# Kernel tuning notes

Measured on AMD Instinct MI355X. Metric: run time of the kernel, lower is better.

## Reference

```python
import jax, jax.numpy as jnp
import numpy as np

# qint16 range and intermediate reciprocal scale (from Div.__init__):
# table_scale = 2 / 0.01 / (qmax - qmin) -> max representable ~ 1/0.01 = 100
QMIN, QMAX = -32768.0, 32767.0
TABLE_SCALE = 2.0 / 0.01 / 65535.0
N_TABLE = 256  # entries per LUT
DENSE = (0.01, 1.0)
SPARSE = (1.0, 7.0)
LLINE = (1e-5, 0.01)
RLINE = (7.0, 20.0)


def _quant(y):
    # quantize a float reciprocal value into the symmetric qint16 table domain
    return jnp.clip(jnp.round(y / TABLE_SCALE), QMIN, QMAX)


def _build_table(xmin, xmax):
    xs = jnp.linspace(xmin, xmax, N_TABLE, dtype=jnp.float32)
    return _quant(1.0 / xs)  # [N_TABLE] quantized reciprocal values


def _lookup(table, ax, xmin, xmax):
    step = (xmax - xmin) / (N_TABLE - 1)
    idx = jnp.clip(jnp.round((ax - xmin) / step), 0, N_TABLE - 1).astype(jnp.int32)
    return table[idx]


def _line(ax, x0, x1):
    # linear fit of reciprocal between the two segment endpoints, then quantize
    y0, y1 = 1.0 / x0, 1.0 / x1
    return _quant(y0 + (ax - x0) * (y1 - y0) / (x1 - x0))


def setup_inputs() -> dict:
    key = jax.random.key(0)
    k1, k2 = jax.random.split(key)
    shape = (4, 16, 1024, 1024)
    data1_q = jax.random.randint(k1, shape, -32768, 32768, dtype=jnp.int32)
    data2_q = jax.random.randint(k2, shape, -32768, 32768, dtype=jnp.int32)
    return {
        "data1_q": data1_q,
        "data2_q": data2_q,
        "data1_scale": jnp.array(1e-3, dtype=jnp.float32),
        "data2_scale": jnp.array(2e-4, dtype=jnp.float32),
        "out_scale": jnp.array(1e-3, dtype=jnp.float32),
    }


def reference(data1_q, data2_q, data1_scale, data2_scale, out_scale):
    # --- multi-table reciprocal on dequantized divisor (symmetric) ---
    x2 = data2_q.astype(jnp.float32) * data2_scale
    sign = jnp.where(x2 >= 0.0, 1.0, -1.0)
    ax = jnp.abs(x2)

    dense_t = _build_table(*DENSE)
    sparse_t = _build_table(*SPARSE)

    recip_q = jnp.where(
        ax < LLINE[0], _quant(1.0 / LLINE[0]),                  # left constant (saturates)
        jnp.where(ax < DENSE[0], _line(ax, *LLINE),             # left line segment
        jnp.where(ax < SPARSE[0], _lookup(dense_t, ax, *DENSE), # dense table
        jnp.where(ax < RLINE[0], _lookup(sparse_t, ax, *SPARSE),# sparse table
        jnp.where(ax < RLINE[1], _line(ax, *RLINE),             # right line segment
                  _quant(1.0 / RLINE[1]))))))                    # right constant
    recip_q = sign * recip_q  # symmetric extension, zero_point = 0

    # --- quantized mul: (data1 * reciprocal) requantized to out_scale ---
    prod = data1_q.astype(jnp.float32) * data1_scale * (recip_q * TABLE_SCALE)
    out_q = jnp.clip(jnp.round(prod / out_scale), QMIN, QMAX)
    return out_q  # int16 repr of QTensor(out_q, out_scale, 'qint16'), as float32
```

## Files before the change

### kernel.cpp

```cpp
#include <hip/hip_runtime.h>


#define TS64     (2.0 / 0.01 / 65535.0)
#define STEPD    (0.99 / 255.0)
#define STEPS    (6.0 / 255.0)
#define INVSTEPD (1.0 / (0.99 / 255.0))
#define INVSTEPS (1.0 / (6.0 / 255.0))

__device__ __forceinline__ void build_tables(double* tbl) {
    const int t = threadIdx.x;
    if (t < 256) {
        double pd = (double)t * STEPD;
        double ps = (double)t * STEPS;
        asm volatile("" : "+v"(pd));
        asm volatile("" : "+v"(ps));
        double xd = 0.01 + pd;
        double xs = 1.0 + ps;
        if (t == 255) { xd = 1.0; xs = 7.0; }
        double qd = rint((1.0 / xd) / TS64);
        double qs = rint((1.0 / xs) / TS64);
        tbl[t]       = fmin(fmax(qd, -32768.0), 32767.0);
        tbl[t + 256] = fmin(fmax(qs, -32768.0), 32767.0);
    }
    __syncthreads();
}

__device__ __forceinline__ float div_elem(int q1i, int q2i, double s2d, double Kd,
                                          const double* tbl) {
    const double ax = fabs((double)q2i * s2d);
    const bool dense = ax < 1.0;
    const double xmin = dense ? 0.01 : 1.0;
    const double inv  = dense ? INVSTEPD : INVSTEPS;
    double idxd = rint((ax - xmin) * inv);
    idxd = fmin(fmax(idxd, 0.0), 255.0);
    double rq = tbl[(int)idxd + (dense ? 0 : 256)];

    if (__builtin_expect(!(ax >= 0.01 && ax < 7.0), 0)) {
        if (ax < 0.01) {
            rq = 32767.0;
        } else if (ax < 20.0) {
            const double y0 = 1.0 / 7.0;
            const double dy = 0.05 - 1.0 / 7.0;
            double y = y0 + (ax - 7.0) * dy / 13.0;
            rq = fmin(fmax(rint(y / TS64), -32768.0), 32767.0);
        } else {
            rq = 16.0;
        }
    }
    rq = (q2i < 0) ? -rq : rq;
    double o = rint((double)q1i * Kd * rq);
    o = fmin(fmax(o, -32768.0), 32767.0);
    return (float)o;
}

__global__ void __launch_bounds__(256)
div_q16_vec4(const int4* __restrict__ q1, const int4* __restrict__ q2,
             const float* __restrict__ s1p, const float* __restrict__ s2p,
             const float* __restrict__ osp, float4* __restrict__ out, int nvec) {
    __shared__ double tbl[512];
    build_tables(tbl);
    const double s2d = (double)s2p[0];
    const double Kd  = (double)s1p[0] * TS64 / (double)osp[0];
    const int stride = gridDim.x * blockDim.x;
    for (int i = blockIdx.x * blockDim.x + threadIdx.x; i < nvec; i += stride) {
        const int4 a = q1[i];
        const int4 b = q2[i];
        float4 o;
        o.x = div_elem(a.x, b.x, s2d, Kd, tbl);
        o.y = div_elem(a.y, b.y, s2d, Kd, tbl);
        o.z = div_elem(a.z, b.z, s2d, Kd, tbl);
        o.w = div_elem(a.w, b.w, s2d, Kd, tbl);
        out[i] = o;
    }
}

__global__ void __launch_bounds__(256)
div_q16_tail(const int* __restrict__ q1, const int* __restrict__ q2,
             const float* __restrict__ s1p, const float* __restrict__ s2p,
             const float* __restrict__ osp, float* __restrict__ out,
             int base, int n) {
    __shared__ double tbl[512];
    build_tables(tbl);
    const double s2d = (double)s2p[0];
    const double Kd  = (double)s1p[0] * TS64 / (double)osp[0];
    const int i = base + blockIdx.x * (int)blockDim.x + threadIdx.x;
    if (i < n) out[i] = div_elem(q1[i], q2[i], s2d, Kd, tbl);
}

extern "C" void kernel_launch(void* const* d_in, const int* in_sizes, int n_in,
                              void* d_out, int out_size, void* d_ws, size_t ws_size,
                              hipStream_t stream) {
    const int n = in_sizes[0];
    const int* q1 = (const int*)d_in[0];
    const int* q2 = (const int*)d_in[1];
    const float* s1 = (const float*)d_in[2];
    const float* s2 = (const float*)d_in[3];
    const float* os = (const float*)d_in[4];
    float* out = (float*)d_out;

    const int nvec = n >> 2;
    const int block = 256;
    if (nvec > 0) {
        int grid = (nvec + block - 1) / block;
        if (grid > 2048) grid = 2048;
        div_q16_vec4<<<grid, block, 0, stream>>>(
            (const int4*)q1, (const int4*)q2, s1, s2, os, (float4*)out, nvec);
    }
    const int tail = n & 3;
    if (tail) {
        div_q16_tail<<<1, block, 0, stream>>>(q1, q2, s1, s2, os, out,
                                              n - tail, n);
    }
}
```

Measured before the change: 163.8 us.

## Replace per-element reciprocal evaluation with per-block 32K-entry integer-indexed LUT

Each block now builds a 32768-entry ushort LDS table that maps |q2| straight to the quantized reciprocal. The per-element fp64 arithmetic (dense/sparse index computation, line segments) becomes one LDS load, and the requantize multiply drops to fp32. Each block pays for building a 64KB table, computing 32 entries per thread in fp64 with a division. Block size goes to 1024 and the grid is capped at 512, which lowers occupancy. Using fp32 for the product may round some results differently from the fp64 path.

```diff
diff --git a/kernel.cpp b/kernel.cpp
--- a/kernel.cpp
+++ b/kernel.cpp
@@ -1,90 +1,88 @@
 #include <hip/hip_runtime.h>
 
 
-#define TS64     (2.0 / 0.01 / 65535.0)
-#define STEPD    (0.99 / 255.0)
-#define STEPS    (6.0 / 255.0)
-#define INVSTEPD (1.0 / (0.99 / 255.0))
-#define INVSTEPS (1.0 / (6.0 / 255.0))
+#define TS64  (2.0 / 0.01 / 65535.0)
+#define STEPD (0.99 / 255.0)
+#define STEPS (6.0 / 255.0)
 
-__device__ __forceinline__ void build_tables(double* tbl) {
-    const int t = threadIdx.x;
-    if (t < 256) {
-        double pd = (double)t * STEPD;
-        double ps = (double)t * STEPS;
-        asm volatile("" : "+v"(pd));
-        asm volatile("" : "+v"(ps));
-        double xd = 0.01 + pd;
-        double xs = 1.0 + ps;
-        if (t == 255) { xd = 1.0; xs = 7.0; }
-        double qd = rint((1.0 / xd) / TS64);
-        double qs = rint((1.0 / xs) / TS64);
-        tbl[t]       = fmin(fmax(qd, -32768.0), 32767.0);
-        tbl[t + 256] = fmin(fmax(qs, -32768.0), 32767.0);
+__device__ __forceinline__ double quant64(double y) {
+    return fmin(fmax(rint(y / TS64), -32768.0), 32767.0);
+}
+
+__device__ double rq_of_aq(int aq, double s2d) {
+    const double ax = (double)aq * s2d;
+    double rq;
+    if (ax < 0.01) {
+        rq = 32767.0;
+    } else if (ax < 7.0) {
+        const bool dense = ax < 1.0;
+        const double xmin = dense ? 0.01 : 1.0;
+        const double step = dense ? STEPD : STEPS;
+        double idx = rint((ax - xmin) / step);
+        idx = fmin(fmax(idx, 0.0), 255.0);
+        double xs;
+        if (idx == 255.0) {
+            xs = dense ? 1.0 : 7.0;
+        } else {
+            double p = idx * step;
+            asm volatile("" : "+v"(p));
+            xs = xmin + p;
+        }
+        rq = quant64(1.0 / xs);
+    } else if (ax < 20.0) {
+        rq = quant64(1.0 / 7.0 + (ax - 7.0) * ((0.05 - 1.0 / 7.0) / 13.0));
+    } else {
+        rq = 16.0;
     }
+    return rq;
+}
+
+__device__ __forceinline__ void build_lut(unsigned short* tbl, const float* s2p) {
+    const double s2d = (double)s2p[0];
+    for (int t = threadIdx.x; t < 32768; t += (int)blockDim.x)
+        tbl[t] = (unsigned short)(int)rq_of_aq(t, s2d);
     __syncthreads();
 }
 
-__device__ __forceinline__ float div_elem(int q1i, int q2i, double s2d, double Kd,
-                                          const double* tbl) {
-    const double ax = fabs((double)q2i * s2d);
-    const bool dense = ax < 1.0;
-    const double xmin = dense ? 0.01 : 1.0;
-    const double inv  = dense ? INVSTEPD : INVSTEPS;
-    double idxd = rint((ax - xmin) * inv);
-    idxd = fmin(fmax(idxd, 0.0), 255.0);
-    double rq = tbl[(int)idxd + (dense ? 0 : 256)];
-
-    if (__builtin_expect(!(ax >= 0.01 && ax < 7.0), 0)) {
-        if (ax < 0.01) {
-            rq = 32767.0;
-        } else if (ax < 20.0) {
-            const double y0 = 1.0 / 7.0;
-            const double dy = 0.05 - 1.0 / 7.0;
-            double y = y0 + (ax - 7.0) * dy / 13.0;
-            rq = fmin(fmax(rint(y / TS64), -32768.0), 32767.0);
-        } else {
-            rq = 16.0;
-        }
-    }
-    rq = (q2i < 0) ? -rq : rq;
-    double o = rint((double)q1i * Kd * rq);
-    o = fmin(fmax(o, -32768.0), 32767.0);
-    return (float)o;
+__device__ __forceinline__ float elem(int a, int b, float kf,
+                                      const unsigned short* tbl) {
+    const int aq = min(abs(b), 32767);
+    float rq = (float)tbl[aq];
+    rq = (b < 0) ? -rq : rq;
+    const float o = rintf((float)a * kf * rq);
+    return fminf(fmaxf(o, -32768.0f), 32767.0f);
 }
 
-__global__ void __launch_bounds__(256)
-div_q16_vec4(const int4* __restrict__ q1, const int4* __restrict__ q2,
+__global__ void __launch_bounds__(1024)
+div_q16_main(const int4* __restrict__ q1, const int4* __restrict__ q2,
              const float* __restrict__ s1p, const float* __restrict__ s2p,
              const float* __restrict__ osp, float4* __restrict__ out, int nvec) {
-    __shared__ double tbl[512];
-    build_tables(tbl);
-    const double s2d = (double)s2p[0];
-    const double Kd  = (double)s1p[0] * TS64 / (double)osp[0];
+    __shared__ unsigned short tbl[32768];
+    build_lut(tbl, s2p);
+    const float kf = (float)((double)s1p[0] * TS64 / (double)osp[0]);
     const int stride = gridDim.x * blockDim.x;
     for (int i = blockIdx.x * blockDim.x + threadIdx.x; i < nvec; i += stride) {
         const int4 a = q1[i];
         const int4 b = q2[i];
         float4 o;
-        o.x = div_elem(a.x, b.x, s2d, Kd, tbl);
-        o.y = div_elem(a.y, b.y, s2d, Kd, tbl);
-        o.z = div_elem(a.z, b.z, s2d, Kd, tbl);
-        o.w = div_elem(a.w, b.w, s2d, Kd, tbl);
+        o.x = elem(a.x, b.x, kf, tbl);
+        o.y = elem(a.y, b.y, kf, tbl);
+        o.z = elem(a.z, b.z, kf, tbl);
+        o.w = elem(a.w, b.w, kf, tbl);
         out[i] = o;
     }
 }
 
-__global__ void __launch_bounds__(256)
+__global__ void __launch_bounds__(1024)
 div_q16_tail(const int* __restrict__ q1, const int* __restrict__ q2,
              const float* __restrict__ s1p, const float* __restrict__ s2p,
              const float* __restrict__ osp, float* __restrict__ out,
              int base, int n) {
-    __shared__ double tbl[512];
-    build_tables(tbl);
-    const double s2d = (double)s2p[0];
-    const double Kd  = (double)s1p[0] * TS64 / (double)osp[0];
+    __shared__ unsigned short tbl[32768];
+    build_lut(tbl, s2p);
+    const float kf = (float)((double)s1p[0] * TS64 / (double)osp[0]);
     const int i = base + blockIdx.x * (int)blockDim.x + threadIdx.x;
-    if (i < n) out[i] = div_elem(q1[i], q2[i], s2d, Kd, tbl);
+    if (i < n) out[i] = elem(q1[i], q2[i], kf, tbl);
 }
 
 extern "C" void kernel_launch(void* const* d_in, const int* in_sizes, int n_in,
@@ -99,11 +97,11 @@
     float* out = (float*)d_out;
 
     const int nvec = n >> 2;
-    const int block = 256;
+    const int block = 1024;
     if (nvec > 0) {
         int grid = (nvec + block - 1) / block;
-        if (grid > 2048) grid = 2048;
-        div_q16_vec4<<<grid, block, 0, stream>>>(
+        if (grid > 512) grid = 512;
+        div_q16_main<<<grid, block, 0, stream>>>(
             (const int4*)q1, (const int4*)q2, s1, s2, os, (float4*)out, nvec);
     }
     const int tail = n & 3;
```

Result: slower. 180.7 us (+10.3%).
